# Kernel optimization log

Hardware: AMD Instinct MI355X
Metric: run time of the kernel (lower is better)

The kernel has to match this reference:

```python
import jax, jax.numpy as jnp
import numpy as np

N = 131072      # number of RoIs (instances)
D = 1024        # in_channels
H = 1024        # hidden dim (hard-coded in module)
L = 4           # number of FPN levels / routed experts
STD = 0.01      # init std for all weights (biases zero)


def setup_inputs() -> dict:
    key = jax.random.key(0)
    k = jax.random.split(key, 5)
    x = jax.random.normal(k[0], (N, D), dtype=jnp.float32)
    levels = jax.random.randint(k[1], (N,), 0, L, dtype=jnp.int32)
    # Per-level MLP params, normal(std=0.01) weights, zero biases.
    W1 = jax.random.normal(k[2], (L, D, H), dtype=jnp.float32) * STD
    b1 = jnp.zeros((L, H), dtype=jnp.float32)
    W2 = jax.random.normal(k[3], (L, H, H), dtype=jnp.float32) * STD
    b2 = jnp.zeros((L, H), dtype=jnp.float32)
    W3 = jax.random.normal(k[4], (L, H, 1), dtype=jnp.float32) * STD
    b3 = jnp.zeros((L, 1), dtype=jnp.float32)
    return {"x": x, "levels": levels, "W1": W1, "b1": b1,
            "W2": W2, "b2": b2, "W3": W3, "b3": b3}


def reference(x, levels, W1, b1, W2, b2, W3, b3):
    # Hard-routed per-level 3-layer MLP (FC-ReLU x2 + FC), dropout in eval
    # mode (identity). Rows routed to level l get that level's MLP output;
    # implemented jit-compatibly with a fixed loop over the 4 levels and a
    # row mask instead of data-dependent gather/scatter.
    result = jnp.zeros((x.shape[0], 1), dtype=x.dtype)
    for lvl in range(L):
        h = jax.nn.relu(x @ W1[lvl] + b1[lvl])       # [N, H]
        h = jax.nn.relu(h @ W2[lvl] + b2[lvl])       # [N, H]
        out = h @ W3[lvl] + b3[lvl]                  # [N, 1]
        result = jnp.where((levels == lvl)[:, None], out, result)
    return result
```

## Files before the change

### kernel.cpp

```cpp
#include <hip/hip_runtime.h>

#define NROWS   131072
#define KDIM    1024
#define NLVL    4
#define SLOT_CAP 132096
#define NSB     516

#define OFF_IDX  1024ull
#define OFF_PART (OFF_IDX + (size_t)SLOT_CAP * 4)
#define OFF_WT1  (OFF_PART + (size_t)SLOT_CAP * 64)
#define OFF_WT2  (OFF_WT1 + 8388608ull)
#define OFF_XBF  (OFF_WT2 + 8388608ull)
#define OFF_H1   (OFF_XBF + 268435456ull)

typedef __bf16 bf16x8 __attribute__((ext_vector_type(8)));
typedef float f32x4 __attribute__((ext_vector_type(4)));
typedef unsigned short u16x4 __attribute__((ext_vector_type(4)));

__device__ __forceinline__ unsigned short f2bf(float f) {
  unsigned int u = __float_as_uint(f);
  u += 0x7fffu + ((u >> 16) & 1u);
  return (unsigned short)(u >> 16);
}

__device__ __forceinline__ void gld_lds16(const void* g, void* l) {
  __builtin_amdgcn_global_load_lds(
      (const __attribute__((address_space(1))) void*)g,
      (__attribute__((address_space(3))) void*)l, 16, 0, 0);
}


__global__ void k_hist(const int* __restrict__ levels, int n, int* __restrict__ meta) {
  __shared__ int h[NLVL];
  if (threadIdx.x < NLVL) h[threadIdx.x] = 0;
  __syncthreads();
  for (int t = blockIdx.x * blockDim.x + threadIdx.x; t < n; t += gridDim.x * blockDim.x)
    atomicAdd(&h[levels[t]], 1);
  __syncthreads();
  if (threadIdx.x < NLVL) atomicAdd(&meta[threadIdx.x], h[threadIdx.x]);
}

__global__ void k_seg(int* meta) {
  if (threadIdx.x == 0 && blockIdx.x == 0) {
    int s = 0;
    for (int l = 0; l < NLVL; ++l) {
      int pc = (meta[l] + 255) & ~255;
      meta[8 + l] = s;
      meta[12 + l] = pc;
      s += pc;
    }
  }
}

__global__ void k_scatter(const int* __restrict__ levels, int n,
                          int* __restrict__ meta, int* __restrict__ idx) {
  __shared__ int h[NLVL], base[NLVL], cur[NLVL];
  int t = blockIdx.x * blockDim.x + threadIdx.x;
  if (threadIdx.x < NLVL) { h[threadIdx.x] = 0; cur[threadIdx.x] = 0; }
  __syncthreads();
  int lvl = 0;
  if (t < n) { lvl = levels[t]; atomicAdd(&h[lvl], 1); }
  __syncthreads();
  if (threadIdx.x < NLVL)
    base[threadIdx.x] = atomicAdd(&meta[4 + threadIdx.x], h[threadIdx.x]);
  __syncthreads();
  if (t < n) {
    int p = atomicAdd(&cur[lvl], 1);
    idx[meta[8 + lvl] + base[lvl] + p] = t;
  }
}

__global__ void k_cvt_x(const f32x4* __restrict__ x, u16x4* __restrict__ xb, int n4) {
  for (int t = blockIdx.x * blockDim.x + threadIdx.x; t < n4; t += gridDim.x * blockDim.x) {
    f32x4 v = x[t];
    u16x4 o;
    o[0] = f2bf(v[0]); o[1] = f2bf(v[1]); o[2] = f2bf(v[2]); o[3] = f2bf(v[3]);
    xb[t] = o;
  }
}

__global__ void k_twt(const float* __restrict__ W, unsigned short* __restrict__ Wt) {
  __shared__ float tile[32][33];
  int lvl = blockIdx.z;
  int k0 = blockIdx.x * 32, n0 = blockIdx.y * 32;
  int tx = threadIdx.x, ty = threadIdx.y;
  const float* Wp = W + (size_t)lvl * 1048576;
  unsigned short* Wtp = Wt + (size_t)lvl * 1048576;
#pragma unroll
  for (int i = 0; i < 4; ++i)
    tile[ty + i * 8][tx] = Wp[(size_t)(k0 + ty + i * 8) * 1024 + n0 + tx];
  __syncthreads();
#pragma unroll
  for (int i = 0; i < 4; ++i) {
    int nn = ty + i * 8;
    Wtp[(size_t)(n0 + nn) * 1024 + k0 + tx] = f2bf(tile[tx][nn]);
  }
}

#define BARR __builtin_amdgcn_s_barrier()
#define WAIT_L  asm volatile("s_waitcnt lgkmcnt(0)" ::: "memory")
#define WAIT_V6 asm volatile("s_waitcnt vmcnt(6) lgkmcnt(0)" ::: "memory")
#define PRIO(x) __builtin_amdgcn_s_setprio(x)

#define RD_W(pi,kk) { const char* p_ = lds + (((pi)*4 + (kk)) << 14) + offW0; \
  wf[0] = *(const bf16x8*)(p_);        wf[1] = *(const bf16x8*)(p_ + 1024);  \
  wf[2] = *(const bf16x8*)(p_ + 2048); wf[3] = *(const bf16x8*)(p_ + 3072); }
#define RD_X(pi,kk,mh) { const char* p_ = lds + (((pi)*4 + 2 + (kk)) << 14) + offX0 + (mh)*4096; \
  xf[0] = *(const bf16x8*)(p_);        xf[1] = *(const bf16x8*)(p_ + 1024);  \
  xf[2] = *(const bf16x8*)(p_ + 2048); xf[3] = *(const bf16x8*)(p_ + 3072); }
#define MMA(mh) { _Pragma("unroll") for (int nf_ = 0; nf_ < 4; ++nf_) { \
  _Pragma("unroll") for (int j_ = 0; j_ < 4; ++j_) \
    acc[nf_][(mh)*4 + j_] = __builtin_amdgcn_mfma_f32_16x16x32_bf16(wf[nf_], xf[j_], acc[nf_][(mh)*4 + j_], 0, 0, 0); } }

template <int PASS>
__global__ __launch_bounds__(512, 2) void k_gemm(
    const unsigned short* __restrict__ Asrc,
    const unsigned short* __restrict__ Wt,
    const float* __restrict__ bias,
    const float* __restrict__ w3,
    const int* __restrict__ meta,
    const int* __restrict__ idx,
    unsigned short* __restrict__ hout,
    float* __restrict__ partial) {
  __shared__ __align__(16) char lds[131072];

  const int bid = blockIdx.x;
  const int swz = (bid & 7) * (NSB * 4 / 8) + (bid >> 3);
  const int nb = swz & 3;
  const int sb = swz >> 2;
  const int slotbase = sb * 256;
  if (slotbase >= meta[11] + meta[15]) return;
  int lvl;
  if      (slotbase < meta[9])  lvl = 0;
  else if (slotbase < meta[10]) lvl = 1;
  else if (slotbase < meta[11]) lvl = 2;
  else                          lvl = 3;

  const int tid = threadIdx.x;
  const int ln  = tid & 63;
  const int w   = tid >> 6;
  const int wn  = w & 3;
  const int wm  = w >> 2;
  const int l15 = ln & 15;

  const int rr0 = w * 16 + (ln >> 2);
  const int cch = (ln & 3) ^ ((rr0 >> 1) & 3);
  int ar0, ar1;
  if (PASS == 1) { ar0 = idx[slotbase + rr0]; ar1 = idx[slotbase + rr0 + 128]; }
  else           { ar0 = slotbase + rr0;      ar1 = slotbase + rr0 + 128; }
  const char* xs0 = (const char*)Asrc + (size_t)ar0 * 2048 + cch * 16;
  const char* xs1 = (const char*)Asrc + (size_t)ar1 * 2048 + cch * 16;
  const char* wlv = (const char*)Wt + ((size_t)lvl << 21);
  const char* ws0 = wlv + (size_t)(nb * 256 + rr0) * 2048 + cch * 16;
  const char* ws1 = ws0 + 128 * 2048;

  auto STG = [&](int t, int isX, int kkh) {
    char* db = (char*)lds + (((t & 1) * 4 + isX * 2 + kkh) << 14) + (w << 10);
    const char* s0 = isX ? xs0 : ws0;
    const char* s1 = isX ? xs1 : ws1;
    const int o = t * 128 + kkh * 64;
    gld_lds16(s0 + o, db);
    gld_lds16(s1 + o, db + 8192);
  };

  const int xorc  = ((ln >> 4) ^ ((l15 >> 1) & 3)) * 16;
  const int offW0 = (wn * 64 + l15) * 64 + xorc;
  const int offX0 = (wm * 128 + l15) * 64 + xorc;

  const f32x4 vzero = {0.f, 0.f, 0.f, 0.f};
  f32x4 acc[4][8];
#pragma unroll
  for (int a = 0; a < 4; ++a)
#pragma unroll
    for (int b = 0; b < 8; ++b) acc[a][b] = vzero;
  bf16x8 wf[4], xf[4];

  STG(0, 0, 0); STG(0, 1, 0); STG(0, 0, 1); STG(0, 1, 1);
  STG(1, 0, 0); STG(1, 1, 0); STG(1, 0, 1);
  asm volatile("s_waitcnt vmcnt(6)" ::: "memory");
  BARR;

  for (int i = 0; i < 8; ++i) {
    const int t0 = 2 * i, t1 = 2 * i + 1;
    const bool g = (i < 7);
    RD_W(0, 0); RD_X(0, 0, 0); STG(t1, 1, 1);
    BARR; WAIT_L; PRIO(1); MMA(0); PRIO(0); BARR;
    RD_X(0, 0, 1); if (g) STG(t0 + 2, 0, 0);
    BARR; WAIT_L; PRIO(1); MMA(1); PRIO(0); BARR;
    RD_W(0, 1); RD_X(0, 1, 0); if (g) STG(t0 + 2, 1, 0);
    BARR; WAIT_L; PRIO(1); MMA(0); PRIO(0); BARR;
    RD_X(0, 1, 1); if (g) STG(t0 + 2, 0, 1);
    BARR; WAIT_V6; PRIO(1); MMA(1); PRIO(0); BARR;
    RD_W(1, 0); RD_X(1, 0, 0); if (g) STG(t0 + 2, 1, 1);
    BARR; WAIT_L; PRIO(1); MMA(0); PRIO(0); BARR;
    RD_X(1, 0, 1); if (g) STG(t1 + 2, 0, 0);
    BARR; WAIT_L; PRIO(1); MMA(1); PRIO(0); BARR;
    RD_W(1, 1); RD_X(1, 1, 0); if (g) STG(t1 + 2, 1, 0);
    BARR; WAIT_L; PRIO(1); MMA(0); PRIO(0); BARR;
    RD_X(1, 1, 1); if (g) STG(t1 + 2, 0, 1);
    BARR; WAIT_V6; PRIO(1); MMA(1); PRIO(0); BARR;
  }

  const float* bv = bias + lvl * 1024;
  const int n_lo = (ln >> 4) * 4;

  if (PASS == 1) {
#pragma unroll
    for (int nf = 0; nf < 4; ++nf) {
#pragma unroll
      for (int mf = 0; mf < 8; ++mf) {
        int slot = slotbase + wm * 128 + mf * 16 + l15;
        int col = nb * 256 + wn * 64 + nf * 16 + n_lo;
        f32x4 bb = *(const f32x4*)&bv[col];
        f32x4 v = acc[nf][mf];
        u16x4 o;
#pragma unroll
        for (int r = 0; r < 4; ++r) o[r] = f2bf(fmaxf(v[r] + bb[r], 0.f));
        *(u16x4*)&hout[(size_t)slot * 1024 + col] = o;
      }
    }
  } else {
    const float* w3v = w3 + lvl * 1024;
    float ps[8] = {0.f, 0.f, 0.f, 0.f, 0.f, 0.f, 0.f, 0.f};
#pragma unroll
    for (int mf = 0; mf < 8; ++mf) {
#pragma unroll
      for (int nf = 0; nf < 4; ++nf) {
        int col = nb * 256 + wn * 64 + nf * 16 + n_lo;
        f32x4 bb = *(const f32x4*)&bv[col];
        f32x4 ww = *(const f32x4*)&w3v[col];
        f32x4 v = acc[nf][mf];
#pragma unroll
        for (int r = 0; r < 4; ++r) ps[mf] += fmaxf(v[r] + bb[r], 0.f) * ww[r];
      }
    }
#pragma unroll
    for (int mf = 0; mf < 8; ++mf) {
      float p = ps[mf];
      p += __shfl_xor(p, 16);
      p += __shfl_xor(p, 32);
      if (ln < 16) {
        int slot = slotbase + wm * 128 + mf * 16 + ln;
        partial[(size_t)slot * 16 + nb * 4 + wn] = p;
      }
    }
  }
}

__global__ void k_final(const int* __restrict__ meta, const int* __restrict__ idx,
                        const float* __restrict__ partial, const float* __restrict__ b3,
                        float* __restrict__ out) {
  int t = blockIdx.x * blockDim.x + threadIdx.x;
  int total = meta[11] + meta[15];
  if (t >= total) return;
  int lvl;
  if (t < meta[9]) lvl = 0;
  else if (t < meta[10]) lvl = 1;
  else if (t < meta[11]) lvl = 2;
  else lvl = 3;
  int local = t - meta[8 + lvl];
  if (local >= meta[lvl]) return;
  int row = idx[t];
  const float* pp = partial + (size_t)t * 16;
  float s = 0.f;
#pragma unroll
  for (int j = 0; j < 16; ++j) s += pp[j];
  out[row] = s + b3[lvl];
}

extern "C" void kernel_launch(void* const* d_in, const int* in_sizes, int n_in,
                              void* d_out, int out_size, void* d_ws, size_t ws_size,
                              hipStream_t stream) {
  const float* x      = (const float*)d_in[0];
  const int*   levels = (const int*)d_in[1];
  const float* W1     = (const float*)d_in[2];
  const float* b1     = (const float*)d_in[3];
  const float* W2     = (const float*)d_in[4];
  const float* b2     = (const float*)d_in[5];
  const float* W3     = (const float*)d_in[6];
  const float* b3     = (const float*)d_in[7];
  float* out = (float*)d_out;

  char* ws = (char*)d_ws;
  int* meta = (int*)ws;
  int* idx = (int*)(ws + OFF_IDX);
  float* partial = (float*)(ws + OFF_PART);
  unsigned short* Wt1 = (unsigned short*)(ws + OFF_WT1);
  unsigned short* Wt2 = (unsigned short*)(ws + OFF_WT2);
  unsigned short* xb  = (unsigned short*)(ws + OFF_XBF);
  unsigned short* h1  = (unsigned short*)(ws + OFF_H1);

  hipMemsetAsync(d_ws, 0, OFF_IDX + (size_t)SLOT_CAP * 4, stream);
  k_hist<<<256, 256, 0, stream>>>(levels, NROWS, meta);
  k_seg<<<1, 64, 0, stream>>>(meta);
  k_scatter<<<512, 256, 0, stream>>>(levels, NROWS, meta, idx);
  k_cvt_x<<<2048, 256, 0, stream>>>((const f32x4*)x, (u16x4*)xb, NROWS * (KDIM / 4));
  k_twt<<<dim3(32, 32, 4), dim3(32, 8), 0, stream>>>(W1, Wt1);
  k_twt<<<dim3(32, 32, 4), dim3(32, 8), 0, stream>>>(W2, Wt2);

  k_gemm<1><<<NSB * 4, 512, 0, stream>>>(xb, Wt1, b1, nullptr, meta, idx, h1, nullptr);
  k_gemm<2><<<NSB * 4, 512, 0, stream>>>(h1, Wt2, b2, W3, meta, idx, nullptr, partial);

  k_final<<<516, 256, 0, stream>>>(meta, idx, partial, b3, out);
}
```

Baseline: 811.8 us.

## Shrink GEMM tile to 256x128 with triple-buffered LDS pipeline

```diff
diff --git a/kernel.cpp b/kernel.cpp
--- a/kernel.cpp
+++ b/kernel.cpp
@@ -5,6 +5,7 @@
 #define NLVL    4
 #define SLOT_CAP 132096
 #define NSB     516
+#define NNB     8
 
 #define OFF_IDX  1024ull
 #define OFF_PART (OFF_IDX + (size_t)SLOT_CAP * 4)
@@ -97,20 +98,28 @@
   }
 }
 
-#define BARR __builtin_amdgcn_s_barrier()
+#define BARRM   asm volatile("s_barrier" ::: "memory")
 #define WAIT_L  asm volatile("s_waitcnt lgkmcnt(0)" ::: "memory")
-#define WAIT_V6 asm volatile("s_waitcnt vmcnt(6) lgkmcnt(0)" ::: "memory")
+#define WAIT_V9 asm volatile("s_waitcnt vmcnt(9)" ::: "memory")
+#define WAIT_V6 asm volatile("s_waitcnt vmcnt(6)" ::: "memory")
+#define WAIT_V3 asm volatile("s_waitcnt vmcnt(3)" ::: "memory")
+#define WAIT_V0 asm volatile("s_waitcnt vmcnt(0)" ::: "memory")
 #define PRIO(x) __builtin_amdgcn_s_setprio(x)
 
-#define RD_W(pi,kk) { const char* p_ = lds + (((pi)*4 + (kk)) << 14) + offW0; \
-  wf[0] = *(const bf16x8*)(p_);        wf[1] = *(const bf16x8*)(p_ + 1024);  \
+#define RDW(p,kk) { const char* p_ = lds + (p)*49152 + 32768 + (kk)*8192 + offW; \
+  wf[0] = *(const bf16x8*)(p_);        wf[1] = *(const bf16x8*)(p_ + 1024);     \
   wf[2] = *(const bf16x8*)(p_ + 2048); wf[3] = *(const bf16x8*)(p_ + 3072); }
-#define RD_X(pi,kk,mh) { const char* p_ = lds + (((pi)*4 + 2 + (kk)) << 14) + offX0 + (mh)*4096; \
-  xf[0] = *(const bf16x8*)(p_);        xf[1] = *(const bf16x8*)(p_ + 1024);  \
+#define RDX(p,kk) { const char* p_ = lds + (p)*49152 + (kk)*16384 + offX;       \
+  xf[0] = *(const bf16x8*)(p_);        xf[1] = *(const bf16x8*)(p_ + 1024);     \
   xf[2] = *(const bf16x8*)(p_ + 2048); xf[3] = *(const bf16x8*)(p_ + 3072); }
-#define MMA(mh) { _Pragma("unroll") for (int nf_ = 0; nf_ < 4; ++nf_) { \
-  _Pragma("unroll") for (int j_ = 0; j_ < 4; ++j_) \
-    acc[nf_][(mh)*4 + j_] = __builtin_amdgcn_mfma_f32_16x16x32_bf16(wf[nf_], xf[j_], acc[nf_][(mh)*4 + j_], 0, 0, 0); } }
+#define MMA4 { _Pragma("unroll") for (int nf_ = 0; nf_ < 4; ++nf_) { \
+  _Pragma("unroll") for (int mf_ = 0; mf_ < 4; ++mf_) \
+    acc[nf_][mf_] = __builtin_amdgcn_mfma_f32_16x16x32_bf16(wf[nf_], xf[mf_], acc[nf_][mf_], 0, 0, 0); } }
+#define STGW(p,t,kk) gld_lds16(ws0 + (t)*128 + (kk)*64, \
+  (char*)lds + (p)*49152 + 32768 + (kk)*8192 + (w << 10))
+#define STGX(p,t,kk) { char* d_ = (char*)lds + (p)*49152 + (kk)*16384 + (w << 10); \
+  gld_lds16(xs0 + (t)*128 + (kk)*64, d_); \
+  gld_lds16(xs1 + (t)*128 + (kk)*64, d_ + 8192); }
 
 template <int PASS>
 __global__ __launch_bounds__(512, 2) void k_gemm(
@@ -122,12 +131,12 @@
     const int* __restrict__ idx,
     unsigned short* __restrict__ hout,
     float* __restrict__ partial) {
-  __shared__ __align__(16) char lds[131072];
+  __shared__ __align__(16) char lds[147456];
 
   const int bid = blockIdx.x;
-  const int swz = (bid & 7) * (NSB * 4 / 8) + (bid >> 3);
-  const int nb = swz & 3;
-  const int sb = swz >> 2;
+  const int swz = (bid & 7) * NSB + (bid >> 3);
+  const int nb = swz & 7;
+  const int sb = swz >> 3;
   const int slotbase = sb * 256;
   if (slotbase >= meta[11] + meta[15]) return;
   int lvl;
@@ -139,67 +148,57 @@
   const int tid = threadIdx.x;
   const int ln  = tid & 63;
   const int w   = tid >> 6;
-  const int wn  = w & 3;
-  const int wm  = w >> 2;
+  const int wm  = w & 3;
+  const int wn  = w >> 2;
   const int l15 = ln & 15;
 
-  const int rr0 = w * 16 + (ln >> 2);
-  const int cch = (ln & 3) ^ ((rr0 >> 1) & 3);
+  const int srow = w * 16 + (ln >> 2);
+  const int cch  = (ln & 3) ^ ((srow >> 1) & 3);
   int ar0, ar1;
-  if (PASS == 1) { ar0 = idx[slotbase + rr0]; ar1 = idx[slotbase + rr0 + 128]; }
-  else           { ar0 = slotbase + rr0;      ar1 = slotbase + rr0 + 128; }
+  if (PASS == 1) { ar0 = idx[slotbase + srow]; ar1 = idx[slotbase + srow + 128]; }
+  else           { ar0 = slotbase + srow;      ar1 = slotbase + srow + 128; }
   const char* xs0 = (const char*)Asrc + (size_t)ar0 * 2048 + cch * 16;
   const char* xs1 = (const char*)Asrc + (size_t)ar1 * 2048 + cch * 16;
-  const char* wlv = (const char*)Wt + ((size_t)lvl << 21);
-  const char* ws0 = wlv + (size_t)(nb * 256 + rr0) * 2048 + cch * 16;
-  const char* ws1 = ws0 + 128 * 2048;
-
-  auto STG = [&](int t, int isX, int kkh) {
-    char* db = (char*)lds + (((t & 1) * 4 + isX * 2 + kkh) << 14) + (w << 10);
-    const char* s0 = isX ? xs0 : ws0;
-    const char* s1 = isX ? xs1 : ws1;
-    const int o = t * 128 + kkh * 64;
-    gld_lds16(s0 + o, db);
-    gld_lds16(s1 + o, db + 8192);
-  };
-
-  const int xorc  = ((ln >> 4) ^ ((l15 >> 1) & 3)) * 16;
-  const int offW0 = (wn * 64 + l15) * 64 + xorc;
-  const int offX0 = (wm * 128 + l15) * 64 + xorc;
+  const char* ws0 = (const char*)Wt + ((size_t)lvl << 21)
+                    + (size_t)(nb * 128 + srow) * 2048 + cch * 16;
+
+  const int xorc = ((ln >> 4) ^ ((l15 >> 1) & 3)) * 16;
+  const int offX = wm * 4096 + l15 * 64 + xorc;
+  const int offW = wn * 4096 + l15 * 64 + xorc;
 
   const f32x4 vzero = {0.f, 0.f, 0.f, 0.f};
-  f32x4 acc[4][8];
+  f32x4 acc[4][4];
 #pragma unroll
   for (int a = 0; a < 4; ++a)
 #pragma unroll
-    for (int b = 0; b < 8; ++b) acc[a][b] = vzero;
+    for (int b = 0; b < 4; ++b) acc[a][b] = vzero;
   bf16x8 wf[4], xf[4];
 
-  STG(0, 0, 0); STG(0, 1, 0); STG(0, 0, 1); STG(0, 1, 1);
-  STG(1, 0, 0); STG(1, 1, 0); STG(1, 0, 1);
-  asm volatile("s_waitcnt vmcnt(6)" ::: "memory");
-  BARR;
-
-  for (int i = 0; i < 8; ++i) {
-    const int t0 = 2 * i, t1 = 2 * i + 1;
-    const bool g = (i < 7);
-    RD_W(0, 0); RD_X(0, 0, 0); STG(t1, 1, 1);
-    BARR; WAIT_L; PRIO(1); MMA(0); PRIO(0); BARR;
-    RD_X(0, 0, 1); if (g) STG(t0 + 2, 0, 0);
-    BARR; WAIT_L; PRIO(1); MMA(1); PRIO(0); BARR;
-    RD_W(0, 1); RD_X(0, 1, 0); if (g) STG(t0 + 2, 1, 0);
-    BARR; WAIT_L; PRIO(1); MMA(0); PRIO(0); BARR;
-    RD_X(0, 1, 1); if (g) STG(t0 + 2, 0, 1);
-    BARR; WAIT_V6; PRIO(1); MMA(1); PRIO(0); BARR;
-    RD_W(1, 0); RD_X(1, 0, 0); if (g) STG(t0 + 2, 1, 1);
-    BARR; WAIT_L; PRIO(1); MMA(0); PRIO(0); BARR;
-    RD_X(1, 0, 1); if (g) STG(t1 + 2, 0, 0);
-    BARR; WAIT_L; PRIO(1); MMA(1); PRIO(0); BARR;
-    RD_W(1, 1); RD_X(1, 1, 0); if (g) STG(t1 + 2, 1, 0);
-    BARR; WAIT_L; PRIO(1); MMA(0); PRIO(0); BARR;
-    RD_X(1, 1, 1); if (g) STG(t1 + 2, 0, 1);
-    BARR; WAIT_V6; PRIO(1); MMA(1); PRIO(0); BARR;
-  }
+  STGW(0, 0, 0); STGX(0, 0, 0); STGW(0, 0, 1); STGX(0, 0, 1);
+  STGW(1, 1, 0); STGX(1, 1, 0); STGW(1, 1, 1); STGX(1, 1, 1);
+  WAIT_V6;
+  BARRM;
+
+#pragma unroll
+  for (int t = 0; t < 14; ++t) {
+    const int p  = t % 3;
+    const int ps = (t + 2) % 3;
+    RDW(p, 0); RDX(p, 0);
+    STGW(ps, t + 2, 0); STGX(ps, t + 2, 0);
+    BARRM; WAIT_L; PRIO(1); MMA4; PRIO(0); WAIT_V9; BARRM;
+    RDW(p, 1); RDX(p, 1);
+    STGW(ps, t + 2, 1); STGX(ps, t + 2, 1);
+    BARRM; WAIT_L; PRIO(1); MMA4; PRIO(0); WAIT_V9; BARRM;
+  }
+
+  RDW(2, 0); RDX(2, 0);
+  BARRM; WAIT_L; PRIO(1); MMA4; PRIO(0); WAIT_V6; BARRM;
+  RDW(2, 1); RDX(2, 1);
+  BARRM; WAIT_L; PRIO(1); MMA4; PRIO(0); WAIT_V3; BARRM;
+  RDW(0, 0); RDX(0, 0);
+  BARRM; WAIT_L; PRIO(1); MMA4; PRIO(0); WAIT_V0; BARRM;
+  RDW(0, 1); RDX(0, 1);
+  WAIT_L; PRIO(1); MMA4; PRIO(0);
 
   const float* bv = bias + lvl * 1024;
   const int n_lo = (ln >> 4) * 4;
@@ -208,9 +207,9 @@
 #pragma unroll
     for (int nf = 0; nf < 4; ++nf) {
 #pragma unroll
-      for (int mf = 0; mf < 8; ++mf) {
-        int slot = slotbase + wm * 128 + mf * 16 + l15;
-        int col = nb * 256 + wn * 64 + nf * 16 + n_lo;
+      for (int mf = 0; mf < 4; ++mf) {
+        int slot = slotbase + wm * 64 + mf * 16 + l15;
+        int col = nb * 128 + wn * 64 + nf * 16 + n_lo;
         f32x4 bb = *(const f32x4*)&bv[col];
         f32x4 v = acc[nf][mf];
         u16x4 o;
@@ -221,27 +220,27 @@
     }
   } else {
     const float* w3v = w3 + lvl * 1024;
-    float ps[8] = {0.f, 0.f, 0.f, 0.f, 0.f, 0.f, 0.f, 0.f};
-#pragma unroll
-    for (int mf = 0; mf < 8; ++mf) {
+    float ps4[4] = {0.f, 0.f, 0.f, 0.f};
+#pragma unroll
+    for (int mf = 0; mf < 4; ++mf) {
 #pragma unroll
       for (int nf = 0; nf < 4; ++nf) {
-        int col = nb * 256 + wn * 64 + nf * 16 + n_lo;
+        int col = nb * 128 + wn * 64 + nf * 16 + n_lo;
         f32x4 bb = *(const f32x4*)&bv[col];
         f32x4 ww = *(const f32x4*)&w3v[col];
         f32x4 v = acc[nf][mf];
 #pragma unroll
-        for (int r = 0; r < 4; ++r) ps[mf] += fmaxf(v[r] + bb[r], 0.f) * ww[r];
+        for (int r = 0; r < 4; ++r) ps4[mf] += fmaxf(v[r] + bb[r], 0.f) * ww[r];
       }
     }
 #pragma unroll
-    for (int mf = 0; mf < 8; ++mf) {
-      float p = ps[mf];
+    for (int mf = 0; mf < 4; ++mf) {
+      float p = ps4[mf];
       p += __shfl_xor(p, 16);
       p += __shfl_xor(p, 32);
       if (ln < 16) {
-        int slot = slotbase + wm * 128 + mf * 16 + ln;
-        partial[(size_t)slot * 16 + nb * 4 + wn] = p;
+        int slot = slotbase + wm * 64 + mf * 16 + ln;
+        partial[(size_t)slot * 16 + nb * 2 + wn] = p;
       }
     }
   }
@@ -298,8 +297,8 @@
   k_twt<<<dim3(32, 32, 4), dim3(32, 8), 0, stream>>>(W1, Wt1);
   k_twt<<<dim3(32, 32, 4), dim3(32, 8), 0, stream>>>(W2, Wt2);
 
-  k_gemm<1><<<NSB * 4, 512, 0, stream>>>(xb, Wt1, b1, nullptr, meta, idx, h1, nullptr);
-  k_gemm<2><<<NSB * 4, 512, 0, stream>>>(h1, Wt2, b2, W3, meta, idx, nullptr, partial);
+  k_gemm<1><<<NSB * NNB, 512, 0, stream>>>(xb, Wt1, b1, nullptr, meta, idx, h1, nullptr);
+  k_gemm<2><<<NSB * NNB, 512, 0, stream>>>(h1, Wt2, b2, W3, meta, idx, nullptr, partial);
 
   k_final<<<516, 256, 0, stream>>>(meta, idx, partial, b3, out);
 }
```

New measurement: 958.6 us. 18.1% more time.
